# Kernel tuning notes

Measured on AMD Instinct MI355X. Metric: run time of the kernel, lower is better.

The kernel has to match this reference:

```python
import jax, jax.numpy as jnp
import numpy as np
import math

# Model dims
B, S, D, H = 2, 2048, 1024, 16
DH = D // H  # 64
TAU = 0.2
EPS = 1e-5

# Unit-scaling scale factors (constraint = gmean of fwd/bwd scales)
# Linear: gmean(fan_in**-0.5, fan_out**-0.5) = (fan_in*fan_out)**-0.25
# Matmul (m,k)@(k,n): gmean(k**-0.5, n**-0.5, m**-0.5) = (m*k*n)**(-1/6)
# Softmax over dim n: gmean(n/1.31, n/1.65) (empirical constants from unit_scaling)
# GELU: gmean(1/0.588, 1/0.675)
MM_SCALE = (S * S * DH) ** (-1.0 / 6.0)
SM_SCALE = S / math.sqrt(1.31 * 1.65)
GELU_SCALE = (0.588 * 0.675) ** -0.5
SQRT_TAU = math.sqrt(TAU)
SQRT_1MTAU = math.sqrt(1.0 - TAU)


def u_linear(x, w, b=None):
    fan_out, fan_in = w.shape
    scale = (fan_in * fan_out) ** -0.25
    y = x @ w.T
    if b is not None:
        y = y + b
    return y * scale


def layer_norm(x, w, b):
    m = jnp.mean(x, axis=-1, keepdims=True)
    v = jnp.mean(jnp.square(x - m), axis=-1, keepdims=True)
    return (x - m) * jax.lax.rsqrt(v + EPS) * w + b


def setup_inputs() -> dict:
    key = jax.random.key(0)
    ks = jax.random.split(key, 8)
    return {
        "x": jax.random.normal(ks[0], (B, S, D), jnp.float32),
        "w_qkv": jax.random.normal(ks[1], (3 * D, D), jnp.float32),
        "w_o": jax.random.normal(ks[2], (D, D), jnp.float32),
        "w1": jax.random.normal(ks[3], (4 * D, D), jnp.float32),
        "b1": jnp.zeros((4 * D,), jnp.float32),
        "w2": jax.random.normal(ks[4], (D, 4 * D), jnp.float32),
        "b2": jnp.zeros((D,), jnp.float32),
        "ln1_w": jnp.ones((D,), jnp.float32),
        "ln1_b": jnp.zeros((D,), jnp.float32),
        "ln2_w": jnp.ones((D,), jnp.float32),
        "ln2_b": jnp.zeros((D,), jnp.float32),
    }


def reference(x, w_qkv, w_o, w1, b1, w2, b2, ln1_w, ln1_b, ln2_w, ln2_b):
    # --- MHSA branch (residual_split forward is identity; tau enters at add) ---
    skip = x
    h = layer_norm(x, ln1_w, ln1_b)
    qkv = u_linear(h, w_qkv)  # [B,S,3D]
    # einops 'b s (d z h) -> z b h s d' with z=3, h=H
    qkv = qkv.reshape(B, S, DH, 3, H)
    q = jnp.transpose(qkv[:, :, :, 0, :], (0, 3, 1, 2))  # [B,H,S,DH]
    k = jnp.transpose(qkv[:, :, :, 1, :], (0, 3, 1, 2))
    v = jnp.transpose(qkv[:, :, :, 2, :], (0, 3, 1, 2))
    scores = jnp.einsum("bhsd,bhtd->bhst", q, k) * MM_SCALE
    attn = jax.nn.softmax(scores, axis=-1) * SM_SCALE
    # dropout: eval mode -> identity
    av = jnp.einsum("bhst,bhtd->bhsd", attn, v) * MM_SCALE
    av = jnp.transpose(av, (0, 2, 1, 3)).reshape(B, S, D)  # b h s d -> b s (h d)
    attn_out = u_linear(av, w_o)
    x = SQRT_TAU * attn_out + SQRT_1MTAU * skip  # residual_add

    # --- MLP branch ---
    skip = x
    h = layer_norm(x, ln2_w, ln2_b)
    h = u_linear(h, w1, b1)
    h = jax.nn.gelu(h, approximate=False) * GELU_SCALE
    h = u_linear(h, w2, b2)
    return SQRT_TAU * h + SQRT_1MTAU * skip
```

## Files before the change

kernel.cpp:

```cpp
#include <hip/hip_runtime.h>
#include <hip/hip_bf16.h>
#include <math.h>

typedef __hip_bfloat16 bf16;
typedef __attribute__((ext_vector_type(8))) short short8;
typedef __attribute__((ext_vector_type(4))) float floatx4;

#define B_   2
#define S_   2048
#define D_   1024
#define H_   16
#define DH_  64
#define BS_  4096
#define D3_  3072
#define DF_  4096

__device__ __forceinline__ float tof(float v) { return v; }
__device__ __forceinline__ float tof(bf16 v) { return __bfloat162float(v); }

__device__ __forceinline__ void gload_lds16(const bf16* g, bf16* l) {
  __builtin_amdgcn_global_load_lds(
      (const __attribute__((address_space(1))) unsigned int*)g,
      (__attribute__((address_space(3))) unsigned int*)l, 16, 0, 0);
}

#define VMCNT(n) asm volatile("s_waitcnt vmcnt(" #n ")" ::: "memory")

__global__ __launch_bounds__(256) void cvt_f32_bf16(
    const float* __restrict__ in, bf16* __restrict__ out, int n4) {
  int i = blockIdx.x * 256 + threadIdx.x;
  if (i >= n4) return;
  float4 v = ((const float4*)in)[i];
  bf16 o[4] = {__float2bfloat16(v.x), __float2bfloat16(v.y),
               __float2bfloat16(v.z), __float2bfloat16(v.w)};
  ((ulong1*)out)[i] = *(ulong1*)o;
}

__global__ __launch_bounds__(256) void cvt_all(
    const float* __restrict__ wqkv, const float* __restrict__ wo,
    const float* __restrict__ w1, bf16* __restrict__ wqb,
    bf16* __restrict__ wob, bf16* __restrict__ w1b) {
  const int g = blockIdx.x * 256 + threadIdx.x;
  if (g < 786432) {
    const int n2 = g >> 8;
    const int col = (g & 255) * 4;
    const int z = n2 >> 10, hh = (n2 >> 6) & 15, d = n2 & 63;
    const int n = d * 48 + z * 16 + hh;
    float4 v = *(const float4*)(wqkv + (size_t)n * 1024 + col);
    bf16 o[4] = {__float2bfloat16(v.x), __float2bfloat16(v.y),
                 __float2bfloat16(v.z), __float2bfloat16(v.w)};
    *(unsigned long long*)(wqb + (size_t)n2 * 1024 + col) =
        *(unsigned long long*)o;
  } else if (g < 1048576) {
    const int g2 = g - 786432;
    float4 v = ((const float4*)wo)[g2];
    bf16 o[4] = {__float2bfloat16(v.x), __float2bfloat16(v.y),
                 __float2bfloat16(v.z), __float2bfloat16(v.w)};
    ((unsigned long long*)wob)[g2] = *(unsigned long long*)o;
  } else {
    const int g2 = g - 1048576;
    float4 v = ((const float4*)w1)[g2];
    bf16 o[4] = {__float2bfloat16(v.x), __float2bfloat16(v.y),
                 __float2bfloat16(v.z), __float2bfloat16(v.w)};
    ((unsigned long long*)w1b)[g2] = *(unsigned long long*)o;
  }
}

template <bool FUSE, bool INIT, typename TA, typename TS>
__global__ __launch_bounds__(256) void resid_ln_kernel(
    const TA* __restrict__ a, const TA* __restrict__ a2,
    const TS* __restrict__ skip,
    const float* __restrict__ w, const float* __restrict__ bias,
    bf16* __restrict__ hout, float st, float s1t,
    float* __restrict__ oinit, const float* __restrict__ b2,
    float cb, float cs) {
  const int row = blockIdx.x;
  const int tid = threadIdx.x;
  const int base = tid * 4;
  const size_t roff = (size_t)row * D_;

  float xv[4];
#pragma unroll
  for (int i = 0; i < 4; i++) {
    float v = tof(a[roff + base + i]);
    if (FUSE) v = st * (v + tof(a2[roff + base + i]))
                  + s1t * tof(skip[roff + base + i]);
    xv[i] = v;
  }
  if (INIT) {
#pragma unroll
    for (int i = 0; i < 4; i++)
      oinit[roff + base + i] = cs * xv[i] + cb * b2[base + i];
  }

  float ls = 0.f, lq = 0.f;
#pragma unroll
  for (int i = 0; i < 4; i++) { ls += xv[i]; lq += xv[i] * xv[i]; }

  __shared__ float ssum[256];
  __shared__ float ssq[256];
  ssum[tid] = ls; ssq[tid] = lq;
  __syncthreads();
  for (int off = 128; off > 0; off >>= 1) {
    if (tid < off) { ssum[tid] += ssum[tid + off]; ssq[tid] += ssq[tid + off]; }
    __syncthreads();
  }
  const float mean = ssum[0] * (1.0f / D_);
  const float var  = ssq[0] * (1.0f / D_) - mean * mean;
  const float rstd = rsqrtf(var + 1e-5f);

#pragma unroll
  for (int i = 0; i < 4; i++) {
    float v = (xv[i] - mean) * rstd * w[base + i] + bias[base + i];
    hout[roff + base + i] = __float2bfloat16(v);
  }
}

__global__ __launch_bounds__(256) void reduce_ffn2(
    const bf16* __restrict__ p0, const bf16* __restrict__ p1,
    float* __restrict__ out, float sc) {
  const size_t i = ((size_t)blockIdx.x * 256 + threadIdx.x) * 8;
  short8 a = *(const short8*)(p0 + i);
  short8 b = *(const short8*)(p1 + i);
  bf16 t0[8], t1[8];
  *(short8*)t0 = a; *(short8*)t1 = b;
  float4 o0 = *(float4*)(out + i);
  float4 o1 = *(float4*)(out + i + 4);
#pragma unroll
  for (int e = 0; e < 4; e++) {
    ((float*)&o0)[e] += sc * (__bfloat162float(t0[e]) + __bfloat162float(t1[e]));
    ((float*)&o1)[e] += sc * (__bfloat162float(t0[e + 4]) + __bfloat162float(t1[e + 4]));
  }
  *(float4*)(out + i) = o0;
  *(float4*)(out + i + 4) = o1;
}

template <int EPI, typename TC>
__global__ __launch_bounds__(512, 2) void gemm_mfma256(
    const bf16* __restrict__ A, const bf16* __restrict__ Bw,
    TC* __restrict__ C, int M, int N, int K, float scale,
    const float* __restrict__ bias, float st) {
  __shared__ __align__(16) bf16 As[2][2][128][64];
  __shared__ __align__(16) bf16 Bs[2][2][128][64];

  const int tid = threadIdx.x;
  const int lane = tid & 63;
  const int w = tid >> 6;
  const int wm = w >> 2;
  const int wn = w & 3;
  const int quad = lane >> 4;
  const int l16 = lane & 15;

  const int nbx = N >> 8;
  const int nwg = nbx * (M >> 8);
  int bid = blockIdx.x;
  bid = (bid & 7) * (nwg >> 3) + (bid >> 3);
  const size_t bm = (size_t)(bid / nbx) * 256;
  const size_t bn = (size_t)(bid % nbx) * 256;

  const bf16* gsrc[4][2];
  bf16* ldsp[4][2];
#pragma unroll
  for (int i = 0; i < 2; i++) {
    const int G = tid + i * 512;
    const int cr = G >> 3;
    const int gs8 = ((G & 7) ^ (cr & 7)) * 8;
    const int ra = ((cr >> 6) << 7) + (cr & 63);
    const int rb = ((cr >> 5) << 6) + (cr & 31);
    gsrc[0][i] = A  + (bm + ra) * (size_t)K + gs8;
    gsrc[2][i] = A  + (bm + ra + 64) * (size_t)K + gs8;
    gsrc[1][i] = Bw + (bn + rb) * (size_t)K + gs8;
    gsrc[3][i] = Bw + (bn + rb + 32) * (size_t)K + gs8;
    ldsp[0][i] = &As[0][0][0][0] + G * 8;
    ldsp[2][i] = &As[0][1][0][0] + G * 8;
    ldsp[1][i] = &Bs[0][0][0][0] + G * 8;
    ldsp[3][i] = &Bs[0][1][0][0] + G * 8;
  }

  auto STAGE = [&](int c, int tn) {
    const int boff = (tn & 1) * 16384;
    gload_lds16(gsrc[c][0] + (size_t)tn * 64, ldsp[c][0] + boff);
    gload_lds16(gsrc[c][1] + (size_t)tn * 64, ldsp[c][1] + boff);
  };

  const int ksw0 = (quad ^ (l16 & 7)) * 8;
  const int ksw1 = ((4 + quad) ^ (l16 & 7)) * 8;

  floatx4 acc[8][4];
#pragma unroll
  for (int i = 0; i < 8; i++)
#pragma unroll
    for (int j = 0; j < 4; j++) acc[i][j] = {0.f, 0.f, 0.f, 0.f};

  short8 af[4][2], bv[2][2];

  auto READ_A = [&](int b, int h) {
#pragma unroll
    for (int mf = 0; mf < 4; mf++) {
      const bf16* p = &As[b][h][wm * 64 + mf * 16 + l16][0];
      af[mf][0] = *(const short8*)(p + ksw0);
      af[mf][1] = *(const short8*)(p + ksw1);
    }
  };
  auto READ_B = [&](int b, int bh) {
#pragma unroll
    for (int nf = 0; nf < 2; nf++) {
      const bf16* p = &Bs[b][bh][wn * 32 + nf * 16 + l16][0];
      bv[nf][0] = *(const short8*)(p + ksw0);
      bv[nf][1] = *(const short8*)(p + ksw1);
    }
  };
  auto MFMA16 = [&](int mb, int nb) {
#pragma unroll
    for (int mf = 0; mf < 4; mf++)
#pragma unroll
      for (int nf = 0; nf < 2; nf++) {
        floatx4 c = acc[mb + mf][nb + nf];
        c = __builtin_amdgcn_mfma_f32_16x16x32_bf16(af[mf][0], bv[nf][0], c, 0, 0, 0);
        c = __builtin_amdgcn_mfma_f32_16x16x32_bf16(af[mf][1], bv[nf][1], c, 0, 0, 0);
        acc[mb + mf][nb + nf] = c;
      }
  };

  STAGE(0, 0); STAGE(1, 0); STAGE(2, 0); STAGE(3, 0);
  VMCNT(4);
  __builtin_amdgcn_s_barrier();
  __builtin_amdgcn_sched_barrier(0);

  const int NT = K >> 6;
#pragma unroll 1
  for (int t = 0; t < NT; t++) {
    const int b = t & 1;
    const bool nl = (t + 1 < NT);
    READ_A(b, 0);
    READ_B(b, 0);
    if (nl) STAGE(0, t + 1);
    __builtin_amdgcn_s_barrier();
    __builtin_amdgcn_sched_barrier(0);
    __builtin_amdgcn_s_setprio(1);
    MFMA16(0, 0);
    __builtin_amdgcn_s_setprio(0);
    if (nl) { VMCNT(2); } else { VMCNT(0); }
    __builtin_amdgcn_s_barrier();
    __builtin_amdgcn_sched_barrier(0);
    READ_B(b, 1);
    if (nl) STAGE(1, t + 1);
    __builtin_amdgcn_s_barrier();
    __builtin_amdgcn_sched_barrier(0);
    __builtin_amdgcn_s_setprio(1);
    MFMA16(0, 2);
    __builtin_amdgcn_s_setprio(0);
    __builtin_amdgcn_s_barrier();
    __builtin_amdgcn_sched_barrier(0);
    READ_A(b, 1);
    if (nl) STAGE(2, t + 1);
    __builtin_amdgcn_s_barrier();
    __builtin_amdgcn_sched_barrier(0);
    __builtin_amdgcn_s_setprio(1);
    MFMA16(4, 2);
    __builtin_amdgcn_s_setprio(0);
    __builtin_amdgcn_s_barrier();
    __builtin_amdgcn_sched_barrier(0);
    READ_B(b, 0);
    if (nl) STAGE(3, t + 1);
    __builtin_amdgcn_s_barrier();
    __builtin_amdgcn_sched_barrier(0);
    __builtin_amdgcn_s_setprio(1);
    MFMA16(4, 0);
    __builtin_amdgcn_s_setprio(0);
    if (nl) { VMCNT(4); } else { VMCNT(0); }
    __builtin_amdgcn_s_barrier();
    __builtin_amdgcn_sched_barrier(0);
  }

  float sc_eff = scale;
  if (EPI == 2) sc_eff = (bn < 1024) ? st : scale;
  float bias4[4];
  if (EPI == 1) {
#pragma unroll
    for (int j = 0; j < 4; j++) bias4[j] = bias[bn + wn * 64 + j * 16 + l16];
  }
#pragma unroll
  for (int mi = 0; mi < 8; mi++) {
    const size_t r0 = bm + wm * 128 + (mi >> 2) * 64 + (mi & 3) * 16 + quad * 4;
#pragma unroll
    for (int r = 0; r < 4; r++) {
      const size_t rowoff = (r0 + r) * (size_t)N + bn + wn * 64 + l16;
#pragma unroll
      for (int j = 0; j < 4; j++) {
        float v = acc[mi][j][r];
        if (EPI == 2) {
          ((bf16*)C)[rowoff + j * 16] = __float2bfloat16(v * sc_eff);
        } else {
          float u = (v + bias4[j]) * scale;
          float tt = u * (0.7978845608f + 0.0356774081f * u * u);
          float e = __builtin_amdgcn_exp2f(tt * 2.8853900818f);
          float th = 1.0f - 2.0f * __builtin_amdgcn_rcpf(e + 1.0f);
          ((bf16*)C)[rowoff + j * 16] =
              __float2bfloat16(0.5f * u * (1.0f + th) * st);
        }
      }
    }
  }
}

__global__ __launch_bounds__(512, 2) void gemm_mfma128(
    const bf16* __restrict__ A, const bf16* __restrict__ Bw,
    bf16* __restrict__ C, bf16* __restrict__ C2, int M, int N, int K) {
  __shared__ __align__(16) bf16 As[2][2][128][64];
  __shared__ __align__(16) bf16 Bs[2][2][64][64];

  const int tid = threadIdx.x;
  const int lane = tid & 63;
  const int w = tid >> 6;
  const int wm = w >> 2;
  const int wn = w & 3;
  const int quad = lane >> 4;
  const int l16 = lane & 15;

  const int nbx = N >> 7;
  const int nwg = nbx * (M >> 8) * 2;
  int bid = blockIdx.x;
  bid = (bid & 7) * (nwg >> 3) + (bid >> 3);
  const int split = bid & 1;
  const int tile = bid >> 1;
  const size_t bm = (size_t)(tile / nbx) * 256;
  const size_t bn = (size_t)(tile % nbx) * 128;
  const int lda = K * 2;
  const int koff = split * K;

  const bf16* gA[2][2];
  bf16* lA[2][2];
#pragma unroll
  for (int i = 0; i < 2; i++) {
    const int G = tid + i * 512;
    const int cr = G >> 3;
    const int gs8 = ((G & 7) ^ (cr & 7)) * 8;
    const int ra = ((cr >> 6) << 7) + (cr & 63);
    gA[0][i] = A + (bm + ra) * (size_t)lda + koff + gs8;
    gA[1][i] = A + (bm + ra + 64) * (size_t)lda + koff + gs8;
    lA[0][i] = &As[0][0][0][0] + G * 8;
    lA[1][i] = &As[0][1][0][0] + G * 8;
  }
  const bf16* gB[2];
  bf16* lB[2];
  {
    const int cr = tid >> 3;
    const int gs8 = ((tid & 7) ^ (cr & 7)) * 8;
    gB[0] = Bw + (bn + cr) * (size_t)lda + koff + gs8;
    gB[1] = Bw + (bn + 64 + cr) * (size_t)lda + koff + gs8;
    lB[0] = &Bs[0][0][0][0] + tid * 8;
    lB[1] = &Bs[0][1][0][0] + tid * 8;
  }

  auto STAGE_A = [&](int h, int tn) {
    const int boff = (tn & 1) * 16384;
    gload_lds16(gA[h][0] + (size_t)tn * 64, lA[h][0] + boff);
    gload_lds16(gA[h][1] + (size_t)tn * 64, lA[h][1] + boff);
  };
  auto STAGE_B = [&](int bh, int tn) {
    const int boff = (tn & 1) * 8192;
    gload_lds16(gB[bh] + (size_t)tn * 64, lB[bh] + boff);
  };

  const int ksw0 = (quad ^ (l16 & 7)) * 8;
  const int ksw1 = ((4 + quad) ^ (l16 & 7)) * 8;

  floatx4 acc[8][2];
#pragma unroll
  for (int i = 0; i < 8; i++)
#pragma unroll
    for (int j = 0; j < 2; j++) acc[i][j] = {0.f, 0.f, 0.f, 0.f};

  short8 af[4][2], bv[2][2];

  auto READ_A = [&](int b, int h) {
#pragma unroll
    for (int mf = 0; mf < 4; mf++) {
      const bf16* p = &As[b][h][wm * 64 + mf * 16 + l16][0];
      af[mf][0] = *(const short8*)(p + ksw0);
      af[mf][1] = *(const short8*)(p + ksw1);
    }
  };
  auto READ_BNF = [&](int b, int nf) {
    const bf16* p = &Bs[b][wn >> 1][(wn & 1) * 32 + nf * 16 + l16][0];
    bv[nf][0] = *(const short8*)(p + ksw0);
    bv[nf][1] = *(const short8*)(p + ksw1);
  };
  auto MFMA8 = [&](int mb, int nf) {
#pragma unroll
    for (int mf = 0; mf < 4; mf++) {
      floatx4 c = acc[mb + mf][nf];
      c = __builtin_amdgcn_mfma_f32_16x16x32_bf16(af[mf][0], bv[nf][0], c, 0, 0, 0);
      c = __builtin_amdgcn_mfma_f32_16x16x32_bf16(af[mf][1], bv[nf][1], c, 0, 0, 0);
      acc[mb + mf][nf] = c;
    }
  };

  STAGE_A(0, 0); STAGE_B(0, 0); STAGE_B(1, 0); STAGE_A(1, 0);
  VMCNT(2);
  __builtin_amdgcn_s_barrier();
  __builtin_amdgcn_sched_barrier(0);

  const int NT = K >> 6;
#pragma unroll 1
  for (int t = 0; t < NT; t++) {
    const int b = t & 1;
    const bool nl = (t + 1 < NT);
    READ_A(b, 0);
    READ_BNF(b, 0);
    if (nl) STAGE_A(0, t + 1);
    __builtin_amdgcn_s_barrier();
    __builtin_amdgcn_sched_barrier(0);
    __builtin_amdgcn_s_setprio(1);
    MFMA8(0, 0);
    __builtin_amdgcn_s_setprio(0);
    __builtin_amdgcn_s_barrier();
    __builtin_amdgcn_sched_barrier(0);
    READ_BNF(b, 1);
    if (nl) STAGE_B(0, t + 1);
    __builtin_amdgcn_s_barrier();
    __builtin_amdgcn_sched_barrier(0);
    __builtin_amdgcn_s_setprio(1);
    MFMA8(0, 1);
    __builtin_amdgcn_s_setprio(0);
    if (nl) { VMCNT(3); } else { VMCNT(0); }
    __builtin_amdgcn_s_barrier();
    __builtin_amdgcn_sched_barrier(0);
    READ_A(b, 1);
    if (nl) STAGE_B(1, t + 1);
    __builtin_amdgcn_s_barrier();
    __builtin_amdgcn_sched_barrier(0);
    __builtin_amdgcn_s_setprio(1);
    MFMA8(4, 1);
    __builtin_amdgcn_s_setprio(0);
    __builtin_amdgcn_s_barrier();
    __builtin_amdgcn_sched_barrier(0);
    if (nl) STAGE_A(1, t + 1);
    __builtin_amdgcn_s_barrier();
    __builtin_amdgcn_sched_barrier(0);
    __builtin_amdgcn_s_setprio(1);
    MFMA8(4, 0);
    __builtin_amdgcn_s_setprio(0);
    if (nl) { VMCNT(2); } else { VMCNT(0); }
    __builtin_amdgcn_s_barrier();
    __builtin_amdgcn_sched_barrier(0);
  }

  bf16* dst = split ? C2 : C;
#pragma unroll
  for (int mi = 0; mi < 8; mi++) {
    const size_t r0 = bm + wm * 128 + (mi >> 2) * 64 + (mi & 3) * 16 + quad * 4;
#pragma unroll
    for (int r = 0; r < 4; r++) {
      const size_t rowoff = (r0 + r) * (size_t)N + bn + wn * 32 + l16;
#pragma unroll
      for (int j = 0; j < 2; j++)
        dst[rowoff + j * 16] = __float2bfloat16(acc[mi][j][r]);
    }
  }
}

__global__ __launch_bounds__(512) void flash_attn_mfma(
    const bf16* __restrict__ qkv, bf16* __restrict__ att, float out_scale) {
  const int flat = (blockIdx.z * H_ + blockIdx.y) * (S_ / 128) + blockIdx.x;
  const int g8 = flat & 7, slot = flat >> 3;
  const int hf = g8 * 4 + (slot >> 4);
  const int qb = (slot & 15) * 128;
  const int h = hf & 15, b = hf >> 4;

  const int tid = threadIdx.x;
  const int lane = tid & 63;
  const int wv = tid >> 6;
  const int quad = lane >> 4;
  const int l16 = lane & 15;

  __shared__ __align__(16) bf16 Ks[2][64][64];
  __shared__ __align__(16) bf16 Vt[2][64][72];
  __shared__ __align__(16) bf16 Ps[128][64];

  const bf16* Qb_ = qkv + (size_t)b * S_ * D3_ + h * DH_;
  const bf16* Kb_ = Qb_ + 1024;
  const bf16* Vb_ = Qb_ + 2048;

  short8 bq0, bq1;
  {
    const bf16* qrow = Qb_ + (size_t)(qb + wv * 16 + l16) * D3_ + quad * 8;
    bq0 = *(const short8*)(qrow);
    bq1 = *(const short8*)(qrow + 32);
  }

  float l_part = 0.f;
  floatx4 o[4];
#pragma unroll
  for (int fd = 0; fd < 4; fd++) o[fd] = {0.f, 0.f, 0.f, 0.f};

  const int prow = wv * 16 + l16;
  const int psw = (prow & 7) << 4;
  char* pbase = (char*)&Ps[0][0] + prow * 128;

  const bf16* ksrc =
      Kb_ + (size_t)(tid >> 3) * D3_ + (((tid & 7) ^ ((tid >> 3) & 7)) * 8);
  bf16* kdst = &Ks[0][0][0] + tid * 8;
  const int vj = tid & 63, vd = (tid >> 6) * 8;

  const int ksw0 = (quad ^ (l16 & 7)) * 8;
  const int ksw1 = ((4 + quad) ^ (l16 & 7)) * 8;

  gload_lds16(ksrc, kdst);
  uint4 vreg = *(const uint4*)(Vb_ + (size_t)vj * D3_ + vd);

  int cur = 0;
  for (int t = 0; t < S_ / 64; t++) {
    {
      bf16 tmp[8];
      *(uint4*)tmp = vreg;
#pragma unroll
      for (int e = 0; e < 8; e++) Vt[cur][vd + e][vj] = tmp[e];
    }
    __syncthreads();

    if (t + 1 < S_ / 64) {
      gload_lds16(ksrc + (size_t)(t + 1) * 64 * D3_, kdst + (cur ^ 1) * 4096);
      vreg = *(const uint4*)(Vb_ + (size_t)((t + 1) * 64 + vj) * D3_ + vd);
    }

    float st[4][4];
    __builtin_amdgcn_s_setprio(1);
#pragma unroll
    for (int fk = 0; fk < 4; fk++) {
      const bf16* kp = &Ks[cur][fk * 16 + l16][0];
      short8 ak0 = *(const short8*)(kp + ksw0);
      short8 ak1 = *(const short8*)(kp + ksw1);
      floatx4 acc = {0.f, 0.f, 0.f, 0.f};
      acc = __builtin_amdgcn_mfma_f32_16x16x32_bf16(ak0, bq0, acc, 0, 0, 0);
      acc = __builtin_amdgcn_mfma_f32_16x16x32_bf16(ak1, bq1, acc, 0, 0, 0);
#pragma unroll
      for (int r = 0; r < 4; r++) st[fk][r] = acc[r];
    }
    __builtin_amdgcn_s_setprio(0);

#pragma unroll
    for (int fk = 0; fk < 2; fk++) {
      bf16 pk[4];
#pragma unroll
      for (int r = 0; r < 4; r++) {
        const float p = __builtin_amdgcn_exp2f(st[fk][r]);
        l_part += p;
        pk[r] = __float2bfloat16(p);
      }
      *(uint2*)(pbase + ((fk * 32 + quad * 8) ^ psw)) = *(uint2*)pk;
    }
    short8 ap0 = *(const short8*)(pbase + ((quad * 16) ^ psw));
#pragma unroll
    for (int fk = 2; fk < 4; fk++) {
      bf16 pk[4];
#pragma unroll
      for (int r = 0; r < 4; r++) {
        const float p = __builtin_amdgcn_exp2f(st[fk][r]);
        l_part += p;
        pk[r] = __float2bfloat16(p);
      }
      *(uint2*)(pbase + ((fk * 32 + quad * 8) ^ psw)) = *(uint2*)pk;
    }
    short8 ap1 = *(const short8*)(pbase + ((64 + quad * 16) ^ psw));

    __builtin_amdgcn_s_setprio(1);
#pragma unroll
    for (int fd = 0; fd < 4; fd++) {
      short8 bv0 = *(const short8*)&Vt[cur][fd * 16 + l16][quad * 8];
      short8 bv1 = *(const short8*)&Vt[cur][fd * 16 + l16][32 + quad * 8];
      o[fd] = __builtin_amdgcn_mfma_f32_16x16x32_bf16(ap0, bv0, o[fd], 0, 0, 0);
      o[fd] = __builtin_amdgcn_mfma_f32_16x16x32_bf16(ap1, bv1, o[fd], 0, 0, 0);
    }
    __builtin_amdgcn_s_setprio(0);

    cur ^= 1;
  }

  l_part += __shfl_xor(l_part, 16);
  l_part += __shfl_xor(l_part, 32);
#pragma unroll
  for (int r = 0; r < 4; r++) {
    const float lq = __shfl(l_part, quad * 4 + r, 64);
    const float sc = out_scale / lq;
    const size_t base =
        ((size_t)(b * S_ + qb + wv * 16 + quad * 4 + r)) * D_ + h * DH_;
#pragma unroll
    for (int fd = 0; fd < 4; fd++)
      att[base + fd * 16 + l16] = __float2bfloat16(o[fd][r] * sc);
  }
}

extern "C" void kernel_launch(void* const* d_in, const int* in_sizes, int n_in,
                              void* d_out, int out_size, void* d_ws, size_t ws_size,
                              hipStream_t stream) {
  const float* x     = (const float*)d_in[0];
  const float* w_qkv = (const float*)d_in[1];
  const float* w_o   = (const float*)d_in[2];
  const float* w1    = (const float*)d_in[3];
  const float* b1    = (const float*)d_in[4];
  const float* w2    = (const float*)d_in[5];
  const float* b2    = (const float*)d_in[6];
  const float* ln1w  = (const float*)d_in[7];
  const float* ln1b  = (const float*)d_in[8];
  const float* ln2w  = (const float*)d_in[9];
  const float* ln2b  = (const float*)d_in[10];
  float* out = (float*)d_out;
  bf16* ws  = (bf16*)d_ws;

  bf16* h1   = ws;
  bf16* wqb  = ws + 4194304;
  bf16* wob  = ws + 7340032;
  bf16* qkv  = ws + 8388608;
  bf16* att  = ws + 20971520;
  bf16* w1b  = ws + 25165824;
  bf16* w2b  = ws;
  bf16* Po   = ws + 8388608;
  bf16* h2   = ws + 4194304;
  bf16* g    = ws + 8388608;
  bf16* Pf0  = ws + 4194304;
  bf16* Pf1  = ws + 25165824;

  const float MM_SCALE   = (float)pow((double)S_ * S_ * DH_, -1.0 / 6.0);
  const float SM_SCALE   = (float)((double)S_ / sqrt(1.31 * 1.65));
  const float GELU_SCALE = (float)pow(0.588 * 0.675, -0.5);
  const float SQRT_TAU   = (float)sqrt(0.2);
  const float SQRT_1MT   = (float)sqrt(0.8);
  const float LOG2E      = 1.4426950408889634f;
  const float qkv_scale  = (float)pow((double)D_ * D3_, -0.25);
  const float o_scale    = (float)pow((double)D_ * D_, -0.25);
  const float w1_scale   = (float)pow((double)D_ * DF_, -0.25);
  const float w2_scale   = (float)pow((double)DF_ * D_, -0.25);

  cvt_all<<<8192, 256, 0, stream>>>(w_qkv, w_o, w1, wqb, wob, w1b);
  resid_ln_kernel<false, false, float, float><<<BS_, 256, 0, stream>>>(
      x, nullptr, nullptr, ln1w, ln1b, h1, 0.f, 0.f, nullptr, nullptr, 0.f, 0.f);
  gemm_mfma256<2, bf16><<<dim3(192), 512, 0, stream>>>(
      h1, wqb, qkv, BS_, D3_, D_, qkv_scale, nullptr,
      qkv_scale * MM_SCALE * LOG2E);
  cvt_f32_bf16<<<4096, 256, 0, stream>>>(w2, w2b, D_ * DF_ / 4);
  flash_attn_mfma<<<dim3(S_ / 128, H_, B_), 512, 0, stream>>>(
      qkv, att, SM_SCALE * MM_SCALE);
  gemm_mfma128<<<dim3(256), 512, 0, stream>>>(
      att, wob, Po, Po + (size_t)BS_ * D_, BS_, D_, D_ / 2);
  resid_ln_kernel<true, true, bf16, float><<<BS_, 256, 0, stream>>>(
      Po, Po + (size_t)BS_ * D_, x, ln2w, ln2b, h2,
      SQRT_TAU * o_scale, SQRT_1MT, out, b2, SQRT_TAU * w2_scale, SQRT_1MT);
  gemm_mfma256<1, bf16><<<dim3(256), 512, 0, stream>>>(
      h2, w1b, g, BS_, DF_, D_, w1_scale, b1, GELU_SCALE);
  gemm_mfma128<<<dim3(256), 512, 0, stream>>>(
      g, w2b, Pf0, Pf1, BS_, D_, DF_ / 2);
  reduce_ffn2<<<2048, 256, 0, stream>>>(Pf0, Pf1, out, SQRT_TAU * w2_scale);
}
```

Baseline: 338.7 us.

## Split attention over two KV halves with a separate combine kernel

The flash attention grid doubles: each block processes half of the key/value sequence and writes unnormalized bf16 partial outputs plus per-row sum buffers. A new combine kernel adds the two partials and normalizes by the summed denominators. This works because the softmax uses no running max, so the halves add directly. K moves to a single LDS buffer with an extra barrier, V gets an XOR-swizzled transposed layout to avoid bank conflicts, and the w2 conversion launch is moved after attention. The aim is more blocks for better CU occupancy (512 to 1024), at the cost of extra partial-output traffic, one more launch, and less K prefetch overlap.

```diff
diff --git a/kernel.cpp b/kernel.cpp
--- a/kernel.cpp
+++ b/kernel.cpp
@@ -135,6 +135,24 @@
   *(float4*)(out + i + 4) = o1;
 }
 
+__global__ __launch_bounds__(256) void combine_attn(
+    const bf16* __restrict__ O0, const bf16* __restrict__ O1,
+    const float* __restrict__ l0, const float* __restrict__ l1,
+    bf16* __restrict__ att, float sc) {
+  const size_t i = ((size_t)blockIdx.x * 256 + threadIdx.x) * 8;
+  const int srow = (int)(i >> 10);
+  const int h = (int)(i >> 6) & 15;
+  const float inv = sc / (l0[srow * H_ + h] + l1[srow * H_ + h]);
+  short8 a = *(const short8*)(O0 + i);
+  short8 b = *(const short8*)(O1 + i);
+  bf16 t0[8], t1[8], o[8];
+  *(short8*)t0 = a; *(short8*)t1 = b;
+#pragma unroll
+  for (int e = 0; e < 8; e++)
+    o[e] = __float2bfloat16((tof(t0[e]) + tof(t1[e])) * inv);
+  *(short8*)(att + i) = *(short8*)o;
+}
+
 template <int EPI, typename TC>
 __global__ __launch_bounds__(512, 2) void gemm_mfma256(
     const bf16* __restrict__ A, const bf16* __restrict__ Bw,
@@ -462,11 +480,15 @@
 }
 
 __global__ __launch_bounds__(512) void flash_attn_mfma(
-    const bf16* __restrict__ qkv, bf16* __restrict__ att, float out_scale) {
-  const int flat = (blockIdx.z * H_ + blockIdx.y) * (S_ / 128) + blockIdx.x;
+    const bf16* __restrict__ qkv, bf16* __restrict__ O0,
+    bf16* __restrict__ O1, float* __restrict__ lb0,
+    float* __restrict__ lb1) {
+  const int flat = (blockIdx.z * H_ + blockIdx.y) * 32 + blockIdx.x;
   const int g8 = flat & 7, slot = flat >> 3;
-  const int hf = g8 * 4 + (slot >> 4);
-  const int qb = (slot & 15) * 128;
+  const int hf = g8 * 4 + (slot >> 5);
+  const int rem = slot & 31;
+  const int qb = (rem >> 1) * 128;
+  const int half = rem & 1;
   const int h = hf & 15, b = hf >> 4;
 
   const int tid = threadIdx.x;
@@ -475,13 +497,13 @@
   const int quad = lane >> 4;
   const int l16 = lane & 15;
 
-  __shared__ __align__(16) bf16 Ks[2][64][64];
-  __shared__ __align__(16) bf16 Vt[2][64][72];
+  __shared__ __align__(16) bf16 Ks[64][64];
+  __shared__ __align__(16) bf16 Vt[2][64][64];
   __shared__ __align__(16) bf16 Ps[128][64];
 
   const bf16* Qb_ = qkv + (size_t)b * S_ * D3_ + h * DH_;
-  const bf16* Kb_ = Qb_ + 1024;
-  const bf16* Vb_ = Qb_ + 2048;
+  const bf16* Kb_ = Qb_ + 1024 + (size_t)half * 1024 * D3_;
+  const bf16* Vb_ = Qb_ + 2048 + (size_t)half * 1024 * D3_;
 
   short8 bq0, bq1;
   {
@@ -501,8 +523,9 @@
 
   const bf16* ksrc =
       Kb_ + (size_t)(tid >> 3) * D3_ + (((tid & 7) ^ ((tid >> 3) & 7)) * 8);
-  bf16* kdst = &Ks[0][0][0] + tid * 8;
+  bf16* kdst = &Ks[0][0] + tid * 8;
   const int vj = tid & 63, vd = (tid >> 6) * 8;
+  const int vjg = vj >> 3, vjr = vj & 7;
 
   const int ksw0 = (quad ^ (l16 & 7)) * 8;
   const int ksw1 = ((4 + quad) ^ (l16 & 7)) * 8;
@@ -510,26 +533,24 @@
   gload_lds16(ksrc, kdst);
   uint4 vreg = *(const uint4*)(Vb_ + (size_t)vj * D3_ + vd);
 
-  int cur = 0;
-  for (int t = 0; t < S_ / 64; t++) {
+  const int NT = 1024 / 64;
+#pragma unroll 1
+  for (int t = 0; t < NT; t++) {
+    const int cur = t & 1;
     {
       bf16 tmp[8];
       *(uint4*)tmp = vreg;
 #pragma unroll
-      for (int e = 0; e < 8; e++) Vt[cur][vd + e][vj] = tmp[e];
+      for (int e = 0; e < 8; e++)
+        Vt[cur][vd + e][((vjg ^ e) << 3) | vjr] = tmp[e];
     }
     __syncthreads();
 
-    if (t + 1 < S_ / 64) {
-      gload_lds16(ksrc + (size_t)(t + 1) * 64 * D3_, kdst + (cur ^ 1) * 4096);
-      vreg = *(const uint4*)(Vb_ + (size_t)((t + 1) * 64 + vj) * D3_ + vd);
-    }
-
     float st[4][4];
     __builtin_amdgcn_s_setprio(1);
 #pragma unroll
     for (int fk = 0; fk < 4; fk++) {
-      const bf16* kp = &Ks[cur][fk * 16 + l16][0];
+      const bf16* kp = &Ks[fk * 16 + l16][0];
       short8 ak0 = *(const short8*)(kp + ksw0);
       short8 ak1 = *(const short8*)(kp + ksw1);
       floatx4 acc = {0.f, 0.f, 0.f, 0.f};
@@ -539,6 +560,12 @@
       for (int r = 0; r < 4; r++) st[fk][r] = acc[r];
     }
     __builtin_amdgcn_s_setprio(0);
+    __syncthreads();
+
+    if (t + 1 < NT) {
+      gload_lds16(ksrc + (size_t)(t + 1) * 64 * D3_, kdst);
+      vreg = *(const uint4*)(Vb_ + (size_t)((t + 1) * 64 + vj) * D3_ + vd);
+    }
 
 #pragma unroll
     for (int fk = 0; fk < 2; fk++) {
@@ -568,27 +595,29 @@
     __builtin_amdgcn_s_setprio(1);
 #pragma unroll
     for (int fd = 0; fd < 4; fd++) {
-      short8 bv0 = *(const short8*)&Vt[cur][fd * 16 + l16][quad * 8];
-      short8 bv1 = *(const short8*)&Vt[cur][fd * 16 + l16][32 + quad * 8];
+      const bf16* vp = &Vt[cur][fd * 16 + l16][0];
+      short8 bv0 = *(const short8*)(vp + ksw0);
+      short8 bv1 = *(const short8*)(vp + ksw1);
       o[fd] = __builtin_amdgcn_mfma_f32_16x16x32_bf16(ap0, bv0, o[fd], 0, 0, 0);
       o[fd] = __builtin_amdgcn_mfma_f32_16x16x32_bf16(ap1, bv1, o[fd], 0, 0, 0);
     }
     __builtin_amdgcn_s_setprio(0);
-
-    cur ^= 1;
   }
 
   l_part += __shfl_xor(l_part, 16);
   l_part += __shfl_xor(l_part, 32);
+
+  bf16* Oo = half ? O1 : O0;
+  float* lo = half ? lb1 : lb0;
+  if (quad == 0)
+    lo[(size_t)(b * S_ + qb + wv * 16 + l16) * H_ + h] = l_part;
 #pragma unroll
   for (int r = 0; r < 4; r++) {
-    const float lq = __shfl(l_part, quad * 4 + r, 64);
-    const float sc = out_scale / lq;
     const size_t base =
         ((size_t)(b * S_ + qb + wv * 16 + quad * 4 + r)) * D_ + h * DH_;
 #pragma unroll
     for (int fd = 0; fd < 4; fd++)
-      att[base + fd * 16 + l16] = __float2bfloat16(o[fd][r] * sc);
+      Oo[base + fd * 16 + l16] = __float2bfloat16(o[fd][r]);
   }
 }
 
@@ -613,8 +642,12 @@
   bf16* wqb  = ws + 4194304;
   bf16* wob  = ws + 7340032;
   bf16* qkv  = ws + 8388608;
-  bf16* att  = ws + 20971520;
   bf16* w1b  = ws + 25165824;
+  bf16* Ob0  = ws + 20971520;
+  bf16* Ob1  = ws;
+  float* l0f = (float*)(ws + 4194304);
+  float* l1f = l0f + 65536;
+  bf16* att  = Ob0;
   bf16* w2b  = ws;
   bf16* Po   = ws + 8388608;
   bf16* h2   = ws + 4194304;
@@ -639,9 +672,11 @@
   gemm_mfma256<2, bf16><<<dim3(192), 512, 0, stream>>>(
       h1, wqb, qkv, BS_, D3_, D_, qkv_scale, nullptr,
       qkv_scale * MM_SCALE * LOG2E);
+  flash_attn_mfma<<<dim3(32, H_, B_), 512, 0, stream>>>(
+      qkv, Ob0, Ob1, l0f, l1f);
+  combine_attn<<<2048, 256, 0, stream>>>(
+      Ob0, Ob1, l0f, l1f, att, SM_SCALE * MM_SCALE);
   cvt_f32_bf16<<<4096, 256, 0, stream>>>(w2, w2b, D_ * DF_ / 4);
-  flash_attn_mfma<<<dim3(S_ / 128, H_, B_), 512, 0, stream>>>(
-      qkv, att, SM_SCALE * MM_SCALE);
   gemm_mfma128<<<dim3(256), 512, 0, stream>>>(
       att, wob, Po, Po + (size_t)BS_ * D_, BS_, D_, D_ / 2);
   resid_ln_kernel<true, true, bf16, float><<<BS_, 256, 0, stream>>>(
```

Result: no change. 338.4 us (-0.1%).
